# Kernel optimization log

Hardware: AMD Instinct MI355X
Metric: run time of the kernel (lower is better)

Reference implementation:

```python
import jax, jax.numpy as jnp
import numpy as np

IN_CH, OUT_CH, B, H, W = 32, 64, 8, 256, 256
EPS = 1e-5

SOBEL_X = [[1., 0., -1.], [2., 0., -2.], [1., 0., -1.]]
SOBEL_Y = [[1., 2., 1.], [0., 0., 0.], [-1., -2., -1.]]
LAP = [[0., 1., 0.], [1., -4., 1.], [0., 1., 0.]]

DN = ('NCHW', 'OIHW', 'NCHW')


def conv2d(x, w, b, pad, groups=1):
    y = jax.lax.conv_general_dilated(x, w, (1, 1), [(pad, pad), (pad, pad)],
                                     dimension_numbers=DN, feature_group_count=groups)
    return y + b[None, :, None, None]


def dw_conv(x, k2d):
    # fixed depthwise 3x3 conv, groups=C, padding=1, no bias
    c = x.shape[1]
    kern = jnp.tile(jnp.asarray(k2d, x.dtype)[None, None], (c, 1, 1, 1))  # (C,1,3,3)
    return jax.lax.conv_general_dilated(x, kern, (1, 1), [(1, 1), (1, 1)],
                                        dimension_numbers=DN, feature_group_count=c)


def bn4d(x, p):  # eval-mode BN; x (B,C,H,W), p (4,C) = gamma, beta, mean, var
    g, b, m, v = p
    s = g * jax.lax.rsqrt(v + EPS)
    return (x - m[None, :, None, None]) * s[None, :, None, None] + b[None, :, None, None]


def bn2d(h, p):  # h (B,C)
    g, b, m, v = p
    return (h - m) * (g * jax.lax.rsqrt(v + EPS)) + b


def _bn_params(key, c):
    k1, k2, k3, k4 = jax.random.split(key, 4)
    g = 1.0 + 0.1 * jax.random.normal(k1, (c,), jnp.float32)
    b = 0.1 * jax.random.normal(k2, (c,), jnp.float32)
    m = 0.1 * jax.random.normal(k3, (c,), jnp.float32)
    v = jax.random.uniform(k4, (c,), jnp.float32, 0.5, 1.5)
    return jnp.stack([g, b, m, v])


def setup_inputs() -> dict:
    key = jax.random.key(0)
    ks = jax.random.split(key, 24)
    s = 0.05
    return {
        'x': jax.random.normal(ks[0], (B, IN_CH, H, W), jnp.float32),
        'gate_w1': s * jax.random.normal(ks[1], (IN_CH, IN_CH), jnp.float32),
        'gate_b1': s * jax.random.normal(ks[2], (IN_CH,), jnp.float32),
        'gate_bn': _bn_params(ks[3], IN_CH),
        'gate_w2': s * jax.random.normal(ks[4], (3, IN_CH), jnp.float32),
        'gate_b2': s * jax.random.normal(ks[5], (3,), jnp.float32),
        'mw1': s * jax.random.normal(ks[6], (OUT_CH, IN_CH, 3, 3), jnp.float32),
        'mb1': s * jax.random.normal(ks[7], (OUT_CH,), jnp.float32),
        'mbn1': _bn_params(ks[8], OUT_CH),
        'mw2': s * jax.random.normal(ks[9], (OUT_CH, OUT_CH, 5, 5), jnp.float32),
        'mb2': s * jax.random.normal(ks[10], (OUT_CH,), jnp.float32),
        'mbn2': _bn_params(ks[11], OUT_CH),
        'sxw': s * jax.random.normal(ks[12], (OUT_CH, IN_CH, 5, 5), jnp.float32),
        'sxb': s * jax.random.normal(ks[13], (OUT_CH,), jnp.float32),
        'sxbn': _bn_params(ks[14], OUT_CH),
        'syw': s * jax.random.normal(ks[15], (OUT_CH, IN_CH, 5, 5), jnp.float32),
        'syb': s * jax.random.normal(ks[16], (OUT_CH,), jnp.float32),
        'sybn': _bn_params(ks[17], OUT_CH),
        'lw': s * jax.random.normal(ks[18], (OUT_CH, IN_CH, 5, 5), jnp.float32),
        'lb': s * jax.random.normal(ks[19], (OUT_CH,), jnp.float32),
        'lbn': _bn_params(ks[20], OUT_CH),
    }


def reference(x, gate_w1, gate_b1, gate_bn, gate_w2, gate_b2,
              mw1, mb1, mbn1, mw2, mb2, mbn2,
              sxw, sxb, sxbn, syw, syb, sybn, lw, lb, lbn):
    # gate: GAP -> 1x1 conv -> BN -> tanh -> 1x1 conv -> top-1 one-hot over 3 experts
    gap = x.mean((2, 3))                                   # (B, C_in)
    h = jnp.tanh(bn2d(gap @ gate_w1.T + gate_b1, gate_bn))
    k = h @ gate_w2.T + gate_b2                            # (B, 3)
    oh = jax.nn.one_hot(jnp.argmax(k, axis=1), 3, dtype=x.dtype)  # (B, 3)

    # expert 0: main branch (conv3x3+BN+ReLU -> conv5x5+BN+ReLU)
    main = jax.nn.relu(bn4d(conv2d(x, mw1, mb1, 1), mbn1))
    main = jax.nn.relu(bn4d(conv2d(main, mw2, mb2, 2), mbn2))

    # expert 1: mean of sobel-x and sobel-y branches
    sx = jax.nn.relu(bn4d(conv2d(dw_conv(x, SOBEL_X), sxw, sxb, 2), sxbn))
    sy = jax.nn.relu(bn4d(conv2d(dw_conv(x, SOBEL_Y), syw, syb, 2), sybn))
    sobel = (sx + sy) * 0.5

    # expert 2: laplacian branch
    lap = jax.nn.relu(bn4d(conv2d(dw_conv(x, LAP), lw, lb, 2), lbn))

    # one-hot gated combination (== stack + one_hot mask + sum in the original)
    w = oh[:, :, None, None, None]  # (B, 3, 1, 1, 1)
    return main * w[:, 0] + sobel * w[:, 1] + lap * w[:, 2]
```

## Files before the change

kernel.cpp:

```cpp
#include <hip/hip_runtime.h>

#define BB 8
#define IC 32
#define OC 64
#define HH 256
#define WW 256
#define EPS 1e-5f

typedef __attribute__((ext_vector_type(8))) short bf16x8;
typedef __attribute__((ext_vector_type(4))) float f32x4;

#define XSTR 40
#define YSTR 40

#define WS_GAP   0
#define WS_BIDX  256
#define WS_W1F   264
#define WS_B1F   (WS_W1F + 9216)
#define WS_W2F   (WS_B1F + 64)
#define WS_B2F   (WS_W2F + 51200)
#define WS_SXWT  (WS_B2F + 64)
#define WS_SXBF  (WS_SXWT + 51200)
#define WS_SYWT  (WS_SXBF + 64)
#define WS_SYBF  (WS_SYWT + 51200)
#define WS_LWT   (WS_SYBF + 64)
#define WS_LBF   (WS_LWT + 51200)

__device__ inline unsigned short bf16r(float f) {
    unsigned int u = __float_as_uint(f);
    unsigned int r = (u + 0x7fffu + ((u >> 16) & 1u)) >> 16;
    return (unsigned short)r;
}

__global__ void prep_kernel(const float* __restrict__ mw1, const float* __restrict__ mb1, const float* __restrict__ mbn1,
                            const float* __restrict__ mw2, const float* __restrict__ mb2, const float* __restrict__ mbn2,
                            const float* __restrict__ sxw, const float* __restrict__ sxb, const float* __restrict__ sxbn,
                            const float* __restrict__ syw, const float* __restrict__ syb, const float* __restrict__ sybn,
                            const float* __restrict__ lw,  const float* __restrict__ lb,  const float* __restrict__ lbn,
                            float* __restrict__ ws) {
    int idx = blockIdx.x * 256 + threadIdx.x;

    if (idx < 18432) {
        int j = idx & 7, lane = (idx >> 3) & 63, oct = (idx >> 9) & 1, ht = idx >> 10;
        int t = ht % 9, h = ht / 9;
        int oc = h * 32 + oct * 16 + (lane & 15);
        int ic = (lane >> 4) * 8 + j;
        float s = mbn1[oc] * rsqrtf(mbn1[192 + oc] + EPS);
        ((unsigned short*)(ws + WS_W1F))[idx] = bf16r(mw1[(oc * IC + ic) * 9 + t] * s);
    }
    if (idx < 102400) {
        int j = idx & 7, lane = (idx >> 3) & 63, oct = (idx >> 9) & 3, ht = idx >> 11;
        int t = ht % 25, h = ht / 25;
        int oc = oct * 16 + (lane & 15);
        int ic = h * 32 + (lane >> 4) * 8 + j;
        float s = mbn2[oc] * rsqrtf(mbn2[192 + oc] + EPS);
        ((unsigned short*)(ws + WS_W2F))[idx] = bf16r(mw2[(oc * OC + ic) * 25 + t] * s);
    }
    if (idx < 51200) {
        int oc = idx & 63, k = (idx >> 6) % 25, ic = idx / (25 * 64);
        float ssx = sxbn[oc] * rsqrtf(sxbn[192 + oc] + EPS);
        float ssy = sybn[oc] * rsqrtf(sybn[192 + oc] + EPS);
        float sl  = lbn[oc]  * rsqrtf(lbn[192 + oc]  + EPS);
        ws[WS_SXWT + idx] = sxw[(oc * IC + ic) * 25 + k] * ssx;
        ws[WS_SYWT + idx] = syw[(oc * IC + ic) * 25 + k] * ssy;
        ws[WS_LWT  + idx] = lw [(oc * IC + ic) * 25 + k] * sl;
    }
    if (idx < 64) {
        float s1 = mbn1[idx] * rsqrtf(mbn1[192 + idx] + EPS);
        ws[WS_B1F + idx] = (mb1[idx] - mbn1[128 + idx]) * s1 + mbn1[64 + idx];
        float s2 = mbn2[idx] * rsqrtf(mbn2[192 + idx] + EPS);
        ws[WS_B2F + idx] = (mb2[idx] - mbn2[128 + idx]) * s2 + mbn2[64 + idx];
        float sx = sxbn[idx] * rsqrtf(sxbn[192 + idx] + EPS);
        ws[WS_SXBF + idx] = (sxb[idx] - sxbn[128 + idx]) * sx + sxbn[64 + idx];
        float sy = sybn[idx] * rsqrtf(sybn[192 + idx] + EPS);
        ws[WS_SYBF + idx] = (syb[idx] - sybn[128 + idx]) * sy + sybn[64 + idx];
        float sl = lbn[idx] * rsqrtf(lbn[192 + idx] + EPS);
        ws[WS_LBF + idx] = (lb[idx] - lbn[128 + idx]) * sl + lbn[64 + idx];
    }
}

__global__ void gap_kernel(const float* __restrict__ x, float* __restrict__ ws) {
    int bc = blockIdx.x;
    const float4* p = (const float4*)(x + (size_t)bc * (HH * WW));
    float s = 0.f;
    for (int i = threadIdx.x; i < (HH * WW) / 4; i += 256) {
        float4 v = p[i];
        s += (v.x + v.y) + (v.z + v.w);
    }
    #pragma unroll
    for (int off = 32; off; off >>= 1) s += __shfl_down(s, off, 64);
    __shared__ float red[4];
    int lane = threadIdx.x & 63, w = threadIdx.x >> 6;
    if (lane == 0) red[w] = s;
    __syncthreads();
    if (threadIdx.x == 0)
        ws[WS_GAP + bc] = (red[0] + red[1] + red[2] + red[3]) * (1.f / (HH * WW));
}

__global__ void gate_kernel(const float* __restrict__ w1, const float* __restrict__ b1,
                            const float* __restrict__ gbn,
                            const float* __restrict__ w2, const float* __restrict__ b2,
                            float* __restrict__ ws) {
    __shared__ float hsh[8][32];
    int tid = threadIdx.x;
    int b = tid >> 5, j = tid & 31;
    float acc = b1[j];
    for (int i = 0; i < 32; i++) acc += ws[WS_GAP + b * 32 + i] * w1[j * 32 + i];
    float s = gbn[j] * rsqrtf(gbn[96 + j] + EPS);
    hsh[b][j] = tanhf((acc - gbn[64 + j]) * s + gbn[32 + j]);
    __syncthreads();
    if (tid < 8) {
        float best = -1e30f; int bi = 0;
        for (int c = 0; c < 3; c++) {
            float k = b2[c];
            for (int jj = 0; jj < 32; jj++) k += hsh[tid][jj] * w2[c * 32 + jj];
            if (k > best) { best = k; bi = c; }
        }
        ((int*)ws)[WS_BIDX + tid] = bi;
    }
}

__global__ void __launch_bounds__(256, 2)
main_kernel(const float* __restrict__ x, const float* __restrict__ ws, float* __restrict__ out) {
    __shared__ __align__(16) short xs[484 * XSTR];
    __shared__ __align__(16) short ys[400 * YSTR];

    int b = blockIdx.y;
    if (((const int*)ws)[WS_BIDX + b] != 0) return;
    int tile = blockIdx.x;
    int ty = (tile >> 4) * 16, tx = (tile & 15) * 16;
    int tid = threadIdx.x;
    int w = tid >> 6, lane = tid & 63, n = lane & 15, quad = lane >> 4;

    const float* xb = x + (size_t)b * IC * HH * WW;
    for (int p = tid; p < 484; p += 256) {
        int rr = p / 22, cc = p % 22;
        int gy = ty - 3 + rr, gx = tx - 3 + cc;
        bool v = ((unsigned)gy < HH) && ((unsigned)gx < WW);
        const float* xp = xb + gy * WW + gx;
        short* dst = xs + p * XSTR;
        #pragma unroll
        for (int ic = 0; ic < IC; ic += 4) {
            float f0 = v ? xp[(size_t)(ic + 0) * (HH * WW)] : 0.f;
            float f1 = v ? xp[(size_t)(ic + 1) * (HH * WW)] : 0.f;
            float f2 = v ? xp[(size_t)(ic + 2) * (HH * WW)] : 0.f;
            float f3 = v ? xp[(size_t)(ic + 3) * (HH * WW)] : 0.f;
            uint2 pk;
            pk.x = (unsigned int)bf16r(f0) | ((unsigned int)bf16r(f1) << 16);
            pk.y = (unsigned int)bf16r(f2) | ((unsigned int)bf16r(f3) << 16);
            *(uint2*)(dst + ic) = pk;
        }
    }

    const short* w1v = (const short*)(ws + WS_W1F);
    const bf16x8* w2v = (const bf16x8*)(ws + WS_W2F);

    f32x4 acc2[4][4];
    #pragma unroll
    for (int i = 0; i < 4; i++)
        #pragma unroll
        for (int jj = 0; jj < 4; jj++) acc2[i][jj] = (f32x4){0.f, 0.f, 0.f, 0.f};
    int mrow0 = w * 4;
    int yr0   = w * 5;

    __syncthreads();

    #pragma unroll 1
    for (int h = 0; h < 2; h++) {
        if (h) __syncthreads();

        #pragma unroll
        for (int cg = 0; cg < 2; cg++) {
            int cb = cg * 4;
            f32x4 a1[5][2];
            #pragma unroll
            for (int rr = 0; rr < 5; rr++) {
                a1[rr][0] = (f32x4){0.f, 0.f, 0.f, 0.f};
                a1[rr][1] = (f32x4){0.f, 0.f, 0.f, 0.f};
            }
            #pragma unroll
            for (int dw = 0; dw < 3; dw++) {
                bf16x8 w1f[3][2];
                #pragma unroll
                for (int dh = 0; dh < 3; dh++) {
                    int t = dh * 3 + dw;
                    w1f[dh][0] = *(const bf16x8*)(w1v + (((h * 9 + t) * 2 + 0) * 64 + lane) * 8);
                    w1f[dh][1] = *(const bf16x8*)(w1v + (((h * 9 + t) * 2 + 1) * 64 + lane) * 8);
                }
                bf16x8 bfr[7];
                #pragma unroll
                for (int rI = 0; rI < 7; rI++)
                    bfr[rI] = *(const bf16x8*)(xs + ((yr0 + rI) * 22 + cb + n + dw) * XSTR + quad * 8);
                #pragma unroll
                for (int dh = 0; dh < 3; dh++)
                    #pragma unroll
                    for (int rr = 0; rr < 5; rr++) {
                        a1[rr][0] = __builtin_amdgcn_mfma_f32_16x16x32_bf16(w1f[dh][0], bfr[rr + dh], a1[rr][0], 0, 0, 0);
                        a1[rr][1] = __builtin_amdgcn_mfma_f32_16x16x32_bf16(w1f[dh][1], bfr[rr + dh], a1[rr][1], 0, 0, 0);
                    }
            }
            #pragma unroll
            for (int oct = 0; oct < 2; oct++) {
                float bias1[4];
                #pragma unroll
                for (int r = 0; r < 4; r++)
                    bias1[r] = ws[WS_B1F + h * 32 + oct * 16 + quad * 4 + r];
                #pragma unroll
                for (int rr = 0; rr < 5; rr++) {
                    int yr = yr0 + rr;
                    int gy2 = ty - 2 + yr, gx2 = tx - 2 + cb + n;
                    bool inb = ((unsigned)gy2 < HH) && ((unsigned)gx2 < WW);
                    float v0 = inb ? fmaxf(a1[rr][oct][0] + bias1[0], 0.f) : 0.f;
                    float v1 = inb ? fmaxf(a1[rr][oct][1] + bias1[1], 0.f) : 0.f;
                    float v2 = inb ? fmaxf(a1[rr][oct][2] + bias1[2], 0.f) : 0.f;
                    float v3 = inb ? fmaxf(a1[rr][oct][3] + bias1[3], 0.f) : 0.f;
                    uint2 pk;
                    pk.x = (unsigned int)bf16r(v0) | ((unsigned int)bf16r(v1) << 16);
                    pk.y = (unsigned int)bf16r(v2) | ((unsigned int)bf16r(v3) << 16);
                    *(uint2*)(ys + (yr * 20 + cb + n) * YSTR + oct * 16 + quad * 4) = pk;
                }
            }
        }
        __syncthreads();

        const bf16x8* w2h = w2v + (size_t)h * 100 * 64;
        bf16x8 af[4];
        {
            int base = 0 * 64 + lane;
            af[0] = w2h[base]; af[1] = w2h[base + 64]; af[2] = w2h[base + 128]; af[3] = w2h[base + 192];
        }
        bf16x8 bfr2[8];
        #pragma unroll
        for (int k = 0; k < 25; k++) {
            int dw = k / 5, dh = k % 5;
            if (dh == 0) {
                #pragma unroll
                for (int rI = 0; rI < 8; rI++)
                    bfr2[rI] = *(const bf16x8*)(ys + ((mrow0 + rI) * 20 + n + dw) * YSTR + quad * 8);
            }
            bf16x8 an[4];
            if (k < 24) {
                int kk = k + 1;
                int tn = (kk % 5) * 5 + (kk / 5);
                int base = tn * 4 * 64 + lane;
                an[0] = w2h[base]; an[1] = w2h[base + 64]; an[2] = w2h[base + 128]; an[3] = w2h[base + 192];
            }
            #pragma unroll
            for (int r4 = 0; r4 < 4; r4++) {
                bf16x8 bb = bfr2[r4 + dh];
                acc2[r4][0] = __builtin_amdgcn_mfma_f32_16x16x32_bf16(af[0], bb, acc2[r4][0], 0, 0, 0);
                acc2[r4][1] = __builtin_amdgcn_mfma_f32_16x16x32_bf16(af[1], bb, acc2[r4][1], 0, 0, 0);
                acc2[r4][2] = __builtin_amdgcn_mfma_f32_16x16x32_bf16(af[2], bb, acc2[r4][2], 0, 0, 0);
                acc2[r4][3] = __builtin_amdgcn_mfma_f32_16x16x32_bf16(af[3], bb, acc2[r4][3], 0, 0, 0);
            }
            af[0] = an[0]; af[1] = an[1]; af[2] = an[2]; af[3] = an[3];
        }
    }

    float bias2[4][4];
    #pragma unroll
    for (int oct = 0; oct < 4; oct++)
        #pragma unroll
        for (int r = 0; r < 4; r++)
            bias2[oct][r] = ws[WS_B2F + oct * 16 + quad * 4 + r];

    float* ob = out + (size_t)b * OC * HH * WW;
    #pragma unroll
    for (int r4 = 0; r4 < 4; r4++) {
        int orow = mrow0 + r4;
        #pragma unroll
        for (int oct = 0; oct < 4; oct++) {
            #pragma unroll
            for (int r = 0; r < 4; r++) {
                int oc = oct * 16 + quad * 4 + r;
                float v = fmaxf(acc2[r4][oct][r] + bias2[oct][r], 0.f);
                ob[(size_t)oc * (HH * WW) + (ty + orow) * WW + tx + n] = v;
            }
        }
    }
}

template <int KID>
__global__ void __launch_bounds__(256, 2)
edge_kernel(const float* __restrict__ x, const float* __restrict__ ws, float* __restrict__ out,
            int want, float scale, int accumulate, int wt_off, int bf_off) {
    constexpr float KSX[9] = {1, 0, -1, 2, 0, -2, 1, 0, -1};
    constexpr float KSY[9] = {1, 2, 1, 0, 0, 0, -1, -2, -1};
    constexpr float KLP[9] = {0, 1, 0, 1, -4, 1, 0, 1, 0};

    __shared__ float xsf[8 * 484];
    __shared__ float ysf[8 * 400];
    int b = blockIdx.y;
    if (((const int*)ws)[WS_BIDX + b] != want) return;
    int tile = blockIdx.x;
    int ty = (tile >> 4) * 16, tx = (tile & 15) * 16;
    int tid = threadIdx.x;

    const float* xb = x + (size_t)b * IC * HH * WW;
    const float* wt = ws + wt_off;
    const float* bf = ws + bf_off;

    float acc[8][8];
    #pragma unroll
    for (int o = 0; o < 8; o++)
        #pragma unroll
        for (int j = 0; j < 8; j++) acc[o][j] = 0.f;

    int ocg = tid >> 5;
    int ps  = tid & 31;
    int row = ps >> 1, c0 = (ps & 1) * 8;

    for (int icc = 0; icc < 4; icc++) {
        if (icc) __syncthreads();
        for (int i = tid; i < 8 * 484; i += 256) {
            int ch = i / 484, rem = i % 484, rr = rem / 22, cc = rem % 22;
            int ic = icc * 8 + ch;
            int gy = ty - 3 + rr, gx = tx - 3 + cc;
            float v = 0.f;
            if ((unsigned)gy < HH && (unsigned)gx < WW) v = xb[(size_t)ic * HH * WW + gy * WW + gx];
            xsf[i] = v;
        }
        __syncthreads();
        for (int p = tid; p < 400; p += 256) {
            int r = p / 20, c = p % 20;
            bool inb = ((unsigned)(ty - 2 + r) < HH) && ((unsigned)(tx - 2 + c) < WW);
            #pragma unroll
            for (int ch = 0; ch < 8; ch++) {
                const float* xp = xsf + ch * 484 + r * 22 + c;
                float v = 0.f;
                #pragma unroll
                for (int k = 0; k < 9; k++) {
                    float kv = (KID == 0) ? KSX[k] : (KID == 1) ? KSY[k] : KLP[k];
                    if (kv != 0.f) v += kv * xp[(k / 3) * 22 + (k % 3)];
                }
                ysf[ch * 400 + p] = inb ? v : 0.f;
            }
        }
        __syncthreads();
        for (int ic8 = 0; ic8 < 8; ic8++) {
            const float* yc = ysf + ic8 * 400;
            const float* wbase = wt + ((icc * 8 + ic8) * 25) * 64 + ocg * 8;
            #pragma unroll
            for (int dh = 0; dh < 5; dh++) {
                #pragma unroll
                for (int dw = 0; dw < 5; dw++) {
                    const float* yp = yc + (row + dh) * 20 + c0 + dw;
                    float yv[8];
                    #pragma unroll
                    for (int j = 0; j < 8; j++) yv[j] = yp[j];
                    const float4* wp = (const float4*)(wbase + (dh * 5 + dw) * 64);
                    float4 wa = wp[0], wb = wp[1];
                    float wr[8] = {wa.x, wa.y, wa.z, wa.w, wb.x, wb.y, wb.z, wb.w};
                    #pragma unroll
                    for (int o = 0; o < 8; o++)
                        #pragma unroll
                        for (int j = 0; j < 8; j++) acc[o][j] += wr[o] * yv[j];
                }
            }
        }
    }
    float* ob = out + (size_t)b * OC * HH * WW;
    #pragma unroll
    for (int o = 0; o < 8; o++) {
        int oc = ocg * 8 + o;
        float bb = bf[oc];
        float* op = ob + (size_t)oc * HH * WW + (ty + row) * WW + tx + c0;
        if (accumulate) {
            #pragma unroll
            for (int j = 0; j < 8; j++) op[j] += scale * fmaxf(acc[o][j] + bb, 0.f);
        } else {
            #pragma unroll
            for (int j = 0; j < 8; j++) op[j] = scale * fmaxf(acc[o][j] + bb, 0.f);
        }
    }
}

extern "C" void kernel_launch(void* const* d_in, const int* in_sizes, int n_in,
                              void* d_out, int out_size, void* d_ws, size_t ws_size,
                              hipStream_t stream) {
    const float* x    = (const float*)d_in[0];
    const float* gw1  = (const float*)d_in[1];
    const float* gb1  = (const float*)d_in[2];
    const float* gbn  = (const float*)d_in[3];
    const float* gw2  = (const float*)d_in[4];
    const float* gb2  = (const float*)d_in[5];
    const float* mw1  = (const float*)d_in[6];
    const float* mb1  = (const float*)d_in[7];
    const float* mbn1 = (const float*)d_in[8];
    const float* mw2  = (const float*)d_in[9];
    const float* mb2  = (const float*)d_in[10];
    const float* mbn2 = (const float*)d_in[11];
    const float* sxw  = (const float*)d_in[12];
    const float* sxb  = (const float*)d_in[13];
    const float* sxbn = (const float*)d_in[14];
    const float* syw  = (const float*)d_in[15];
    const float* syb  = (const float*)d_in[16];
    const float* sybn = (const float*)d_in[17];
    const float* lw   = (const float*)d_in[18];
    const float* lb   = (const float*)d_in[19];
    const float* lbn  = (const float*)d_in[20];
    float* ws  = (float*)d_ws;
    float* out = (float*)d_out;

    prep_kernel<<<400, 256, 0, stream>>>(mw1, mb1, mbn1, mw2, mb2, mbn2,
                                         sxw, sxb, sxbn, syw, syb, sybn, lw, lb, lbn, ws);
    gap_kernel<<<256, 256, 0, stream>>>(x, ws);
    gate_kernel<<<1, 256, 0, stream>>>(gw1, gb1, gbn, gw2, gb2, ws);

    dim3 grid(256, BB);
    main_kernel<<<grid, 256, 0, stream>>>(x, ws, out);
    edge_kernel<0><<<grid, 256, 0, stream>>>(x, ws, out, 1, 0.5f, 0, WS_SXWT, WS_SXBF);
    edge_kernel<1><<<grid, 256, 0, stream>>>(x, ws, out, 1, 0.5f, 1, WS_SYWT, WS_SYBF);
    edge_kernel<2><<<grid, 256, 0, stream>>>(x, ws, out, 2, 1.0f, 0, WS_LWT, WS_LBF);
}
```

Measured before the change: 428.5 us.

## Pre-transpose input to channel-last bf16 and load tiles asynchronously into LDS

Adds a transform kernel that converts x into a channel-last bf16 copy in workspace and also computes the GAP with atomics, replacing the separate GAP pass. The main expert kernel then fills its swizzled LDS tile with global_load_lds DMA instead of strided fp32 loads plus conversion. Weight fragments are prefetched four taps ahead in a ring. The three edge kernels are merged into one launch that picks its branch at runtime. This costs an extra 16 MB workspace write and read, depends on the workspace being large enough, and the runtime kernel selection in the edge kernel can hurt code generation.

```diff
diff --git a/kernel.cpp b/kernel.cpp
--- a/kernel.cpp
+++ b/kernel.cpp
@@ -10,8 +10,8 @@
 typedef __attribute__((ext_vector_type(8))) short bf16x8;
 typedef __attribute__((ext_vector_type(4))) float f32x4;
 
+#define YSTR 40
 #define XSTR 40
-#define YSTR 40
 
 #define WS_GAP   0
 #define WS_BIDX  256
@@ -25,11 +25,21 @@
 #define WS_SYBF  (WS_SYWT + 51200)
 #define WS_LWT   (WS_SYBF + 64)
 #define WS_LBF   (WS_LWT + 51200)
+#define WS_XT    (WS_LBF + 64)
+#define WS_ZPAD  (WS_XT + 8388608)
+#define WS_NEED_FAST ((size_t)(WS_ZPAD + 16) * 4)
 
 __device__ inline unsigned short bf16r(float f) {
     unsigned int u = __float_as_uint(f);
     unsigned int r = (u + 0x7fffu + ((u >> 16) & 1u)) >> 16;
     return (unsigned short)r;
+}
+
+__device__ __forceinline__ void gld16(const void* g, const void* l) {
+    __builtin_amdgcn_global_load_lds(
+        (const __attribute__((address_space(1))) void*)(unsigned long long)(g),
+        (__attribute__((address_space(3))) void*)(unsigned int)(unsigned long long)(l),
+        16, 0, 0);
 }
 
 __global__ void prep_kernel(const float* __restrict__ mw1, const float* __restrict__ mb1, const float* __restrict__ mbn1,
@@ -37,7 +47,7 @@
                             const float* __restrict__ sxw, const float* __restrict__ sxb, const float* __restrict__ sxbn,
                             const float* __restrict__ syw, const float* __restrict__ syb, const float* __restrict__ sybn,
                             const float* __restrict__ lw,  const float* __restrict__ lb,  const float* __restrict__ lbn,
-                            float* __restrict__ ws) {
+                            float* __restrict__ ws, int fast) {
     int idx = blockIdx.x * 256 + threadIdx.x;
 
     if (idx < 18432) {
@@ -65,6 +75,8 @@
         ws[WS_SYWT + idx] = syw[(oc * IC + ic) * 25 + k] * ssy;
         ws[WS_LWT  + idx] = lw [(oc * IC + ic) * 25 + k] * sl;
     }
+    if (idx < 256) ws[WS_GAP + idx] = 0.f;
+    if (fast && idx < 16) ws[WS_ZPAD + idx] = 0.f;
     if (idx < 64) {
         float s1 = mbn1[idx] * rsqrtf(mbn1[192 + idx] + EPS);
         ws[WS_B1F + idx] = (mb1[idx] - mbn1[128 + idx]) * s1 + mbn1[64 + idx];
@@ -77,6 +89,40 @@
         float sl = lbn[idx] * rsqrtf(lbn[192 + idx] + EPS);
         ws[WS_LBF + idx] = (lb[idx] - lbn[128 + idx]) * sl + lbn[64 + idx];
     }
+}
+
+__global__ void __launch_bounds__(256, 2)
+xform_kernel(const float* __restrict__ x, float* __restrict__ ws) {
+    int b = blockIdx.y, row = blockIdx.x, t = threadIdx.x;
+    const float* xb = x + (size_t)b * (IC * HH * WW) + (size_t)row * WW;
+
+    unsigned int pk[16];
+    #pragma unroll
+    for (int k = 0; k < 32; k += 2) {
+        float v0 = xb[(size_t)k * (HH * WW) + t];
+        float v1 = xb[(size_t)(k + 1) * (HH * WW) + t];
+        pk[k >> 1] = (unsigned int)bf16r(v0) | ((unsigned int)bf16r(v1) << 16);
+    }
+    short* xt = (short*)(ws + WS_XT) + ((size_t)b * (HH * WW) + (size_t)row * WW + t) * 32;
+    uint4* dp = (uint4*)xt;
+    dp[0] = make_uint4(pk[0],  pk[1],  pk[2],  pk[3]);
+    dp[1] = make_uint4(pk[4],  pk[5],  pk[6],  pk[7]);
+    dp[2] = make_uint4(pk[8],  pk[9],  pk[10], pk[11]);
+    dp[3] = make_uint4(pk[12], pk[13], pk[14], pk[15]);
+
+    __shared__ float gl[32];
+    int w = t >> 6, lane = t & 63;
+    #pragma unroll
+    for (int kk = 0; kk < 8; kk++) {
+        int k = w * 8 + kk;
+        const float* rp = xb + (size_t)k * (HH * WW);
+        float s = rp[lane] + rp[lane + 64] + rp[lane + 128] + rp[lane + 192];
+        #pragma unroll
+        for (int off = 32; off; off >>= 1) s += __shfl_down(s, off, 64);
+        if (lane == 0) gl[k] = s;
+    }
+    __syncthreads();
+    if (t < 32) atomicAdd(ws + WS_GAP + b * 32 + t, gl[t] * (1.f / (HH * WW)));
 }
 
 __global__ void gap_kernel(const float* __restrict__ x, float* __restrict__ ws) {
@@ -120,10 +166,11 @@
     }
 }
 
+template <int ASYNC>
 __global__ void __launch_bounds__(256, 2)
 main_kernel(const float* __restrict__ x, const float* __restrict__ ws, float* __restrict__ out) {
-    __shared__ __align__(16) short xs[484 * XSTR];
-    __shared__ __align__(16) short ys[400 * YSTR];
+    __shared__ __align__(1024) short xs[ASYNC ? 496 * 32 : 484 * XSTR];
+    __shared__ __align__(16)   short ys[400 * YSTR];
 
     int b = blockIdx.y;
     if (((const int*)ws)[WS_BIDX + b] != 0) return;
@@ -132,25 +179,50 @@
     int tid = threadIdx.x;
     int w = tid >> 6, lane = tid & 63, n = lane & 15, quad = lane >> 4;
 
-    const float* xb = x + (size_t)b * IC * HH * WW;
-    for (int p = tid; p < 484; p += 256) {
-        int rr = p / 22, cc = p % 22;
-        int gy = ty - 3 + rr, gx = tx - 3 + cc;
-        bool v = ((unsigned)gy < HH) && ((unsigned)gx < WW);
-        const float* xp = xb + gy * WW + gx;
-        short* dst = xs + p * XSTR;
-        #pragma unroll
-        for (int ic = 0; ic < IC; ic += 4) {
-            float f0 = v ? xp[(size_t)(ic + 0) * (HH * WW)] : 0.f;
-            float f1 = v ? xp[(size_t)(ic + 1) * (HH * WW)] : 0.f;
-            float f2 = v ? xp[(size_t)(ic + 2) * (HH * WW)] : 0.f;
-            float f3 = v ? xp[(size_t)(ic + 3) * (HH * WW)] : 0.f;
-            uint2 pk;
-            pk.x = (unsigned int)bf16r(f0) | ((unsigned int)bf16r(f1) << 16);
-            pk.y = (unsigned int)bf16r(f2) | ((unsigned int)bf16r(f3) << 16);
-            *(uint2*)(dst + ic) = pk;
-        }
-    }
+    if constexpr (ASYNC) {
+        const short* xtb = (const short*)(ws + WS_XT) + (size_t)b * (HH * WW * 32);
+        const void* zp = (const void*)(ws + WS_ZPAD);
+        for (int c = w; c < 31; c += 4) {
+            int D = c * 1024 + (lane << 4);
+            int L = D ^ (((D >> 7) & 7) << 4);
+            int pL = L >> 6, qL = (L >> 4) & 3;
+            int rr = pL / 22, cc2 = pL - rr * 22;
+            int gy = ty - 3 + rr, gx = tx - 3 + cc2;
+            bool v = (pL < 484) && ((unsigned)gy < HH) && ((unsigned)gx < WW);
+            const void* src = v ? (const void*)(xtb + (((gy << 8) + gx) * 32) + (qL << 3)) : zp;
+            gld16(src, (const void*)((const char*)xs + c * 1024));
+        }
+    } else {
+        const float* xb = x + (size_t)b * IC * HH * WW;
+        for (int p = tid; p < 484; p += 256) {
+            int rr = p / 22, cc = p % 22;
+            int gy = ty - 3 + rr, gx = tx - 3 + cc;
+            bool v = ((unsigned)gy < HH) && ((unsigned)gx < WW);
+            const float* xp = xb + gy * WW + gx;
+            short* dst = xs + p * XSTR;
+            #pragma unroll
+            for (int ic = 0; ic < IC; ic += 4) {
+                float f0 = v ? xp[(size_t)(ic + 0) * (HH * WW)] : 0.f;
+                float f1 = v ? xp[(size_t)(ic + 1) * (HH * WW)] : 0.f;
+                float f2 = v ? xp[(size_t)(ic + 2) * (HH * WW)] : 0.f;
+                float f3 = v ? xp[(size_t)(ic + 3) * (HH * WW)] : 0.f;
+                uint2 pk;
+                pk.x = (unsigned int)bf16r(f0) | ((unsigned int)bf16r(f1) << 16);
+                pk.y = (unsigned int)bf16r(f2) | ((unsigned int)bf16r(f3) << 16);
+                *(uint2*)(dst + ic) = pk;
+            }
+        }
+    }
+
+    auto ldb = [&](int P) -> bf16x8 {
+        if constexpr (ASYNC) {
+            int L = (P << 6) + (quad << 4);
+            int A = L ^ (((L >> 7) & 7) << 4);
+            return *(const bf16x8*)((const char*)xs + A);
+        } else {
+            return *(const bf16x8*)(xs + P * XSTR + quad * 8);
+        }
+    };
 
     const short* w1v = (const short*)(ws + WS_W1F);
     const bf16x8* w2v = (const bf16x8*)(ws + WS_W2F);
@@ -190,7 +262,7 @@
                 bf16x8 bfr[7];
                 #pragma unroll
                 for (int rI = 0; rI < 7; rI++)
-                    bfr[rI] = *(const bf16x8*)(xs + ((yr0 + rI) * 22 + cb + n + dw) * XSTR + quad * 8);
+                    bfr[rI] = ldb((yr0 + rI) * 22 + cb + n + dw);
                 #pragma unroll
                 for (int dh = 0; dh < 3; dh++)
                     #pragma unroll
@@ -214,20 +286,23 @@
                     float v1 = inb ? fmaxf(a1[rr][oct][1] + bias1[1], 0.f) : 0.f;
                     float v2 = inb ? fmaxf(a1[rr][oct][2] + bias1[2], 0.f) : 0.f;
                     float v3 = inb ? fmaxf(a1[rr][oct][3] + bias1[3], 0.f) : 0.f;
-                    uint2 pk;
-                    pk.x = (unsigned int)bf16r(v0) | ((unsigned int)bf16r(v1) << 16);
-                    pk.y = (unsigned int)bf16r(v2) | ((unsigned int)bf16r(v3) << 16);
-                    *(uint2*)(ys + (yr * 20 + cb + n) * YSTR + oct * 16 + quad * 4) = pk;
+                    uint2 pkk;
+                    pkk.x = (unsigned int)bf16r(v0) | ((unsigned int)bf16r(v1) << 16);
+                    pkk.y = (unsigned int)bf16r(v2) | ((unsigned int)bf16r(v3) << 16);
+                    *(uint2*)(ys + (yr * 20 + cb + n) * YSTR + oct * 16 + quad * 4) = pkk;
                 }
             }
         }
         __syncthreads();
 
         const bf16x8* w2h = w2v + (size_t)h * 100 * 64;
-        bf16x8 af[4];
-        {
-            int base = 0 * 64 + lane;
-            af[0] = w2h[base]; af[1] = w2h[base + 64]; af[2] = w2h[base + 128]; af[3] = w2h[base + 192];
+        bf16x8 afq[4][4];
+        #pragma unroll
+        for (int kp = 0; kp < 4; kp++) {
+            int tn = (kp % 5) * 5 + (kp / 5);
+            int base = tn * 256 + lane;
+            afq[kp][0] = w2h[base];       afq[kp][1] = w2h[base + 64];
+            afq[kp][2] = w2h[base + 128]; afq[kp][3] = w2h[base + 192];
         }
         bf16x8 bfr2[8];
         #pragma unroll
@@ -238,22 +313,21 @@
                 for (int rI = 0; rI < 8; rI++)
                     bfr2[rI] = *(const bf16x8*)(ys + ((mrow0 + rI) * 20 + n + dw) * YSTR + quad * 8);
             }
-            bf16x8 an[4];
-            if (k < 24) {
-                int kk = k + 1;
-                int tn = (kk % 5) * 5 + (kk / 5);
-                int base = tn * 4 * 64 + lane;
-                an[0] = w2h[base]; an[1] = w2h[base + 64]; an[2] = w2h[base + 128]; an[3] = w2h[base + 192];
-            }
             #pragma unroll
             for (int r4 = 0; r4 < 4; r4++) {
                 bf16x8 bb = bfr2[r4 + dh];
-                acc2[r4][0] = __builtin_amdgcn_mfma_f32_16x16x32_bf16(af[0], bb, acc2[r4][0], 0, 0, 0);
-                acc2[r4][1] = __builtin_amdgcn_mfma_f32_16x16x32_bf16(af[1], bb, acc2[r4][1], 0, 0, 0);
-                acc2[r4][2] = __builtin_amdgcn_mfma_f32_16x16x32_bf16(af[2], bb, acc2[r4][2], 0, 0, 0);
-                acc2[r4][3] = __builtin_amdgcn_mfma_f32_16x16x32_bf16(af[3], bb, acc2[r4][3], 0, 0, 0);
-            }
-            af[0] = an[0]; af[1] = an[1]; af[2] = an[2]; af[3] = an[3];
+                acc2[r4][0] = __builtin_amdgcn_mfma_f32_16x16x32_bf16(afq[k & 3][0], bb, acc2[r4][0], 0, 0, 0);
+                acc2[r4][1] = __builtin_amdgcn_mfma_f32_16x16x32_bf16(afq[k & 3][1], bb, acc2[r4][1], 0, 0, 0);
+                acc2[r4][2] = __builtin_amdgcn_mfma_f32_16x16x32_bf16(afq[k & 3][2], bb, acc2[r4][2], 0, 0, 0);
+                acc2[r4][3] = __builtin_amdgcn_mfma_f32_16x16x32_bf16(afq[k & 3][3], bb, acc2[r4][3], 0, 0, 0);
+            }
+            if (k + 4 < 25) {
+                int kk = k + 4;
+                int tn = (kk % 5) * 5 + (kk / 5);
+                int base = tn * 256 + lane;
+                afq[k & 3][0] = w2h[base];       afq[k & 3][1] = w2h[base + 64];
+                afq[k & 3][2] = w2h[base + 128]; afq[k & 3][3] = w2h[base + 192];
+            }
         }
     }
 
@@ -280,10 +354,8 @@
     }
 }
 
-template <int KID>
 __global__ void __launch_bounds__(256, 2)
-edge_kernel(const float* __restrict__ x, const float* __restrict__ ws, float* __restrict__ out,
-            int want, float scale, int accumulate, int wt_off, int bf_off) {
+edge_kernel(const float* __restrict__ x, const float* __restrict__ ws, float* __restrict__ out) {
     constexpr float KSX[9] = {1, 0, -1, 2, 0, -2, 1, 0, -1};
     constexpr float KSY[9] = {1, 2, 1, 0, 0, 0, -1, -2, -1};
     constexpr float KLP[9] = {0, 1, 0, 1, -4, 1, 0, 1, 0};
@@ -291,86 +363,93 @@
     __shared__ float xsf[8 * 484];
     __shared__ float ysf[8 * 400];
     int b = blockIdx.y;
-    if (((const int*)ws)[WS_BIDX + b] != want) return;
+    int sel = ((const int*)ws)[WS_BIDX + b];
+    if (sel == 0) return;
+    int npass = (sel == 1) ? 2 : 1;
+    float scale = (sel == 1) ? 0.5f : 1.0f;
+
     int tile = blockIdx.x;
     int ty = (tile >> 4) * 16, tx = (tile & 15) * 16;
     int tid = threadIdx.x;
-
     const float* xb = x + (size_t)b * IC * HH * WW;
-    const float* wt = ws + wt_off;
-    const float* bf = ws + bf_off;
-
-    float acc[8][8];
-    #pragma unroll
-    for (int o = 0; o < 8; o++)
-        #pragma unroll
-        for (int j = 0; j < 8; j++) acc[o][j] = 0.f;
 
     int ocg = tid >> 5;
     int ps  = tid & 31;
     int row = ps >> 1, c0 = (ps & 1) * 8;
 
-    for (int icc = 0; icc < 4; icc++) {
-        if (icc) __syncthreads();
-        for (int i = tid; i < 8 * 484; i += 256) {
-            int ch = i / 484, rem = i % 484, rr = rem / 22, cc = rem % 22;
-            int ic = icc * 8 + ch;
-            int gy = ty - 3 + rr, gx = tx - 3 + cc;
-            float v = 0.f;
-            if ((unsigned)gy < HH && (unsigned)gx < WW) v = xb[(size_t)ic * HH * WW + gy * WW + gx];
-            xsf[i] = v;
-        }
-        __syncthreads();
-        for (int p = tid; p < 400; p += 256) {
-            int r = p / 20, c = p % 20;
-            bool inb = ((unsigned)(ty - 2 + r) < HH) && ((unsigned)(tx - 2 + c) < WW);
-            #pragma unroll
-            for (int ch = 0; ch < 8; ch++) {
-                const float* xp = xsf + ch * 484 + r * 22 + c;
+    for (int pass = 0; pass < npass; pass++) {
+        int kid = (sel == 1) ? pass : 2;
+        const float* wt = ws + (kid == 0 ? WS_SXWT : (kid == 1 ? WS_SYWT : WS_LWT));
+        const float* bf = ws + (kid == 0 ? WS_SXBF : (kid == 1 ? WS_SYBF : WS_LBF));
+
+        float acc[8][8];
+        #pragma unroll
+        for (int o = 0; o < 8; o++)
+            #pragma unroll
+            for (int j = 0; j < 8; j++) acc[o][j] = 0.f;
+
+        for (int icc = 0; icc < 4; icc++) {
+            if (icc || pass) __syncthreads();
+            for (int i = tid; i < 8 * 484; i += 256) {
+                int ch = i / 484, rem = i % 484, rr = rem / 22, cc = rem % 22;
+                int ic = icc * 8 + ch;
+                int gy = ty - 3 + rr, gx = tx - 3 + cc;
                 float v = 0.f;
-                #pragma unroll
-                for (int k = 0; k < 9; k++) {
-                    float kv = (KID == 0) ? KSX[k] : (KID == 1) ? KSY[k] : KLP[k];
-                    if (kv != 0.f) v += kv * xp[(k / 3) * 22 + (k % 3)];
+                if ((unsigned)gy < HH && (unsigned)gx < WW) v = xb[(size_t)ic * HH * WW + gy * WW + gx];
+                xsf[i] = v;
+            }
+            __syncthreads();
+            for (int p = tid; p < 400; p += 256) {
+                int r = p / 20, c = p % 20;
+                bool inb = ((unsigned)(ty - 2 + r) < HH) && ((unsigned)(tx - 2 + c) < WW);
+                #pragma unroll
+                for (int ch = 0; ch < 8; ch++) {
+                    const float* xp = xsf + ch * 484 + r * 22 + c;
+                    float v = 0.f;
+                    #pragma unroll
+                    for (int k = 0; k < 9; k++) {
+                        float kv = (kid == 0) ? KSX[k] : (kid == 1) ? KSY[k] : KLP[k];
+                        v += kv * xp[(k / 3) * 22 + (k % 3)];
+                    }
+                    ysf[ch * 400 + p] = inb ? v : 0.f;
                 }
-                ysf[ch * 400 + p] = inb ? v : 0.f;
-            }
-        }
-        __syncthreads();
-        for (int ic8 = 0; ic8 < 8; ic8++) {
-            const float* yc = ysf + ic8 * 400;
-            const float* wbase = wt + ((icc * 8 + ic8) * 25) * 64 + ocg * 8;
-            #pragma unroll
-            for (int dh = 0; dh < 5; dh++) {
-                #pragma unroll
-                for (int dw = 0; dw < 5; dw++) {
-                    const float* yp = yc + (row + dh) * 20 + c0 + dw;
-                    float yv[8];
+            }
+            __syncthreads();
+            for (int ic8 = 0; ic8 < 8; ic8++) {
+                const float* yc = ysf + ic8 * 400;
+                const float* wbase = wt + ((icc * 8 + ic8) * 25) * 64 + ocg * 8;
+                #pragma unroll
+                for (int dh = 0; dh < 5; dh++) {
                     #pragma unroll
-                    for (int j = 0; j < 8; j++) yv[j] = yp[j];
-                    const float4* wp = (const float4*)(wbase + (dh * 5 + dw) * 64);
-                    float4 wa = wp[0], wb = wp[1];
-                    float wr[8] = {wa.x, wa.y, wa.z, wa.w, wb.x, wb.y, wb.z, wb.w};
-                    #pragma unroll
-                    for (int o = 0; o < 8; o++)
+                    for (int dw = 0; dw < 5; dw++) {
+                        const float* yp = yc + (row + dh) * 20 + c0 + dw;
+                        float yv[8];
                         #pragma unroll
-                        for (int j = 0; j < 8; j++) acc[o][j] += wr[o] * yv[j];
+                        for (int j = 0; j < 8; j++) yv[j] = yp[j];
+                        const float4* wp = (const float4*)(wbase + (dh * 5 + dw) * 64);
+                        float4 wa = wp[0], wb = wp[1];
+                        float wr[8] = {wa.x, wa.y, wa.z, wa.w, wb.x, wb.y, wb.z, wb.w};
+                        #pragma unroll
+                        for (int o = 0; o < 8; o++)
+                            #pragma unroll
+                            for (int j = 0; j < 8; j++) acc[o][j] += wr[o] * yv[j];
+                    }
                 }
             }
         }
-    }
-    float* ob = out + (size_t)b * OC * HH * WW;
-    #pragma unroll
-    for (int o = 0; o < 8; o++) {
-        int oc = ocg * 8 + o;
-        float bb = bf[oc];
-        float* op = ob + (size_t)oc * HH * WW + (ty + row) * WW + tx + c0;
-        if (accumulate) {
-            #pragma unroll
-            for (int j = 0; j < 8; j++) op[j] += scale * fmaxf(acc[o][j] + bb, 0.f);
-        } else {
-            #pragma unroll
-            for (int j = 0; j < 8; j++) op[j] = scale * fmaxf(acc[o][j] + bb, 0.f);
+        float* ob = out + (size_t)b * OC * HH * WW;
+        #pragma unroll
+        for (int o = 0; o < 8; o++) {
+            int oc = ocg * 8 + o;
+            float bb = bf[oc];
+            float* op = ob + (size_t)oc * HH * WW + (ty + row) * WW + tx + c0;
+            if (pass) {
+                #pragma unroll
+                for (int j = 0; j < 8; j++) op[j] += scale * fmaxf(acc[o][j] + bb, 0.f);
+            } else {
+                #pragma unroll
+                for (int j = 0; j < 8; j++) op[j] = scale * fmaxf(acc[o][j] + bb, 0.f);
+            }
         }
     }
 }
@@ -402,14 +481,22 @@
     float* ws  = (float*)d_ws;
     float* out = (float*)d_out;
 
+    int fast = (ws_size >= WS_NEED_FAST) ? 1 : 0;
+
     prep_kernel<<<400, 256, 0, stream>>>(mw1, mb1, mbn1, mw2, mb2, mbn2,
-                                         sxw, sxb, sxbn, syw, syb, sybn, lw, lb, lbn, ws);
-    gap_kernel<<<256, 256, 0, stream>>>(x, ws);
+                                         sxw, sxb, sxbn, syw, syb, sybn, lw, lb, lbn, ws, fast);
+    if (fast) {
+        xform_kernel<<<dim3(HH, BB), 256, 0, stream>>>(x, ws);
+    } else {
+        gap_kernel<<<256, 256, 0, stream>>>(x, ws);
+    }
     gate_kernel<<<1, 256, 0, stream>>>(gw1, gb1, gbn, gw2, gb2, ws);
 
     dim3 grid(256, BB);
-    main_kernel<<<grid, 256, 0, stream>>>(x, ws, out);
-    edge_kernel<0><<<grid, 256, 0, stream>>>(x, ws, out, 1, 0.5f, 0, WS_SXWT, WS_SXBF);
-    edge_kernel<1><<<grid, 256, 0, stream>>>(x, ws, out, 1, 0.5f, 1, WS_SYWT, WS_SYBF);
-    edge_kernel<2><<<grid, 256, 0, stream>>>(x, ws, out, 2, 1.0f, 0, WS_LWT, WS_LBF);
-}
+    if (fast) {
+        main_kernel<1><<<grid, 256, 0, stream>>>(x, ws, out);
+    } else {
+        main_kernel<0><<<grid, 256, 0, stream>>>(x, ws, out);
+    }
+    edge_kernel<<<grid, 256, 0, stream>>>(x, ws, out);
+}
```

New measurement: 435.4 us. Within noise of the previous version (+1.6%).
